# Kernel tuning notes

Hardware: AMD Instinct MI355X
Metric: run time of the kernel (lower is better)

The kernel has to match this reference:

```python
import jax, jax.numpy as jnp
import numpy as np

UNITS = 512
SENSORY = 256
BATCH = 256
ODE_UNFOLDS = 6
EPSILON = 1e-8
ELAPSED_TIME = 1.0


def setup_inputs() -> dict:
    key = jax.random.key(0)
    ks = jax.random.split(key, 16)
    u = lambda k, shape, lo, hi: jax.random.uniform(k, shape, jnp.float32, lo, hi)
    pm1 = lambda k, shape: (jax.random.randint(k, shape, 0, 2).astype(jnp.float32) * 2.0 - 1.0)
    return {
        "x": jax.random.normal(ks[0], (BATCH, SENSORY), jnp.float32),
        "state": jax.random.normal(ks[1], (BATCH, UNITS), jnp.float32),
        "gleak": u(ks[2], (UNITS,), 0.001, 1.0),
        "vleak": u(ks[3], (UNITS,), -0.2, 0.2),
        "cm": u(ks[4], (UNITS,), 0.4, 0.6),
        "sigma": u(ks[5], (UNITS, UNITS), 3.0, 8.0),
        "mu": u(ks[6], (UNITS, UNITS), 0.3, 0.8),
        "w": u(ks[7], (UNITS, UNITS), 0.001, 1.0),
        "erev": pm1(ks[8], (UNITS, UNITS)),
        "sensory_sigma": u(ks[9], (SENSORY, UNITS), 3.0, 8.0),
        "sensory_mu": u(ks[10], (SENSORY, UNITS), 0.3, 0.8),
        "sensory_w": u(ks[11], (SENSORY, UNITS), 0.001, 1.0),
        "sensory_erev": pm1(ks[12], (SENSORY, UNITS)),
        "input_w": jnp.ones((SENSORY,), jnp.float32),
        "input_b": jnp.zeros((SENSORY,), jnp.float32),
        "output_w": jnp.ones((UNITS,), jnp.float32),
        "output_b": jnp.zeros((UNITS,), jnp.float32),
    }


def _gate(v_pre, mu, sigma):
    # v_pre: (B, P) broadcast against (P, Q) params -> (B, P, Q)
    return jax.nn.sigmoid(sigma * (v_pre[:, :, None] - mu))


def reference(x, state, gleak, vleak, cm, sigma, mu, w, erev,
              sensory_sigma, sensory_mu, sensory_w, sensory_erev,
              input_w, input_b, output_w, output_b):
    inputs = x * input_w + input_b  # (B, D)
    sens_act = sensory_w * _gate(inputs, sensory_mu, sensory_sigma)  # (B, D, N)
    w_num_sensory = jnp.sum(sens_act * sensory_erev, axis=1)  # (B, N)
    w_den_sensory = jnp.sum(sens_act, axis=1)                 # (B, N)

    cm_t = cm / ((ELAPSED_TIME + 0.001) / ODE_UNFOLDS)  # (N,)
    v_pre = state
    for _ in range(ODE_UNFOLDS):
        w_act = w * _gate(v_pre, mu, sigma)               # (B, N, N)
        w_num = jnp.sum(w_act * erev, axis=1) + w_num_sensory
        w_den = jnp.sum(w_act, axis=1) + w_den_sensory
        numerator = cm_t * v_pre + gleak * vleak + w_num
        denominator = cm_t + gleak + w_den
        v_pre = numerator / (denominator + EPSILON)

    outputs = v_pre * output_w + output_b
    return outputs, v_pre
```

## Files before the change

### kernel.cpp

```cpp
#include <hip/hip_runtime.h>

#define UNITS 512
#define SENSD 256
#define BATCH 256
#define BN (BATCH * UNITS)
#define LOG2E 1.44269504088896340736f
#define CMF (6.0f / 1.001f)

__device__ __forceinline__ float frcp(float x)  { return __builtin_amdgcn_rcpf(x); }
__device__ __forceinline__ float fexp2(float x) { return __builtin_amdgcn_exp2f(x); }

__global__ __launch_bounds__(256) void prep_kernel(
    const float* __restrict__ sigma, const float* __restrict__ mu,
    const float* __restrict__ w, const float* __restrict__ erev,
    const float* __restrict__ ssig, const float* __restrict__ smu,
    const float* __restrict__ sw, const float* __restrict__ serev,
    const float* __restrict__ gleak, const float* __restrict__ vleak,
    const float* __restrict__ cm,
    float4* __restrict__ fusedR, float4* __restrict__ fusedS,
    float4* __restrict__ cmg) {
  int idx = blockIdx.x * 256 + threadIdx.x;
  if (idx < UNITS * UNITS) {
    float s = sigma[idx], m = mu[idx], ww = w[idx], e = erev[idx];
    fusedR[idx] = make_float4(-s * LOG2E, s * m * LOG2E, ww, ww * e);
  } else {
    int j = idx - UNITS * UNITS;
    if (j < SENSD * UNITS) {
      float s = ssig[j], m = smu[j], ww = sw[j], e = serev[j];
      fusedS[j] = make_float4(-s * LOG2E, s * m * LOG2E, ww, ww * e);
    }
  }
  if (idx < UNITS) {
    float cmt = cm[idx] * CMF, gl = gleak[idx];
    cmg[idx] = make_float4(cmt, gl * vleak[idx], cmt + gl + 1e-8f, 0.f);
  }
}

__global__ __launch_bounds__(256, 2) void sensory_kernel(
    const float* __restrict__ x, const float* __restrict__ in_w, const float* __restrict__ in_b,
    const float4* __restrict__ fusedS,
    float* __restrict__ snf, float* __restrict__ sdf) {
  __shared__ float xl[128][20];
  int bi = blockIdx.x;
  int phs = bi & 1, qt = (bi >> 1) & 7, bt = bi >> 4;
  int tid = threadIdx.x;
  for (int i = tid; i < 2048; i += 256) {
    int br = i >> 7, dl = i & 127;
    int d = phs * 128 + dl;
    xl[dl][br] = fmaf(x[(bt * 16 + br) * SENSD + d], in_w[d], in_b[d]);
  }
  __syncthreads();
  int ql = tid & 63, bg = tid >> 6;
  int q = qt * 64 + ql;
  int r0 = bg * 4;
  const float4* F = fusedS + (size_t)(phs * 128) * UNITS + q;
  float n0 = 0.f, n1 = 0.f, n2 = 0.f, n3 = 0.f;
  float d0 = 0.f, d1 = 0.f, d2 = 0.f, d3 = 0.f;
  #pragma unroll 8
  for (int dd = 0; dd < 128; ++dd) {
    float4 f = F[(size_t)dd * UNITS];
    float4 vv = *(const float4*)&xl[dd][r0];
    float t0 = fexp2(fmaf(f.x, vv.x, f.y));
    float t1 = fexp2(fmaf(f.x, vv.y, f.y));
    float t2 = fexp2(fmaf(f.x, vv.z, f.y));
    float t3 = fexp2(fmaf(f.x, vv.w, f.y));
    float s0 = frcp(1.0f + t0);
    float s1 = frcp(1.0f + t1);
    float s2 = frcp(1.0f + t2);
    float s3 = frcp(1.0f + t3);
    n0 = fmaf(f.w, s0, n0);  d0 = fmaf(f.z, s0, d0);
    n1 = fmaf(f.w, s1, n1);  d1 = fmaf(f.z, s1, d1);
    n2 = fmaf(f.w, s2, n2);  d2 = fmaf(f.z, s2, d2);
    n3 = fmaf(f.w, s3, n3);  d3 = fmaf(f.z, s3, d3);
  }
  int bp = (bt * 16 + r0) * UNITS + q;
  size_t o = (size_t)phs * BN + bp;
  snf[o] = n0;             sdf[o] = d0;
  snf[o + UNITS] = n1;     sdf[o + UNITS] = d1;
  snf[o + 2 * UNITS] = n2; sdf[o + 2 * UNITS] = d2;
  snf[o + 3 * UNITS] = n3; sdf[o + 3 * UNITS] = d3;
}

__global__ __launch_bounds__(256, 2) void unfold_kernel(
    const float4* __restrict__ fusedR, const float* __restrict__ vprev,
    const float* __restrict__ pn_in, const float* __restrict__ pd_in,
    const float* __restrict__ snf, const float* __restrict__ sdf,
    const float4* __restrict__ cmg,
    float* __restrict__ vout,
    float* __restrict__ pn_out, float* __restrict__ pd_out,
    int first) {
  __shared__ float vl[128][20];
  int bi = blockIdx.x;
  int ph = bi & 3, qt = (bi >> 2) & 7, bt = bi >> 5;
  int tid = threadIdx.x;
  if (first) {
    for (int i = tid; i < 2048; i += 256) {
      int br = i >> 7, pl = i & 127;
      vl[pl][br] = vprev[(bt * 16 + br) * UNITS + ph * 128 + pl];
    }
  } else {
    for (int i = tid; i < 2048; i += 256) {
      int br = i >> 7, pl = i & 127;
      int p = ph * 128 + pl;
      int bp = (bt * 16 + br) * UNITS + p;
      float num = ((pn_in[bp] + pn_in[BN + bp]) + (pn_in[2 * BN + bp] + pn_in[3 * BN + bp]))
                + (snf[bp] + snf[BN + bp]);
      float den = ((pd_in[bp] + pd_in[BN + bp]) + (pd_in[2 * BN + bp] + pd_in[3 * BN + bp]))
                + (sdf[bp] + sdf[BN + bp]);
      float4 c = cmg[p];
      float v = fmaf(c.x, vprev[bp], c.y + num) * frcp(c.z + den);
      vl[pl][br] = v;
      if (qt == 0) vout[bp] = v;
    }
  }
  __syncthreads();
  int ql = tid & 63, bg = tid >> 6;
  int q = qt * 64 + ql;
  int r0 = bg * 4;
  const float4* F = fusedR + (size_t)(ph * 128) * UNITS + q;
  float n0 = 0.f, n1 = 0.f, n2 = 0.f, n3 = 0.f;
  float d0 = 0.f, d1 = 0.f, d2 = 0.f, d3 = 0.f;
  #pragma unroll 8
  for (int pp = 0; pp < 128; ++pp) {
    float4 f = F[(size_t)pp * UNITS];
    float4 vv = *(const float4*)&vl[pp][r0];
    float t0 = fexp2(fmaf(f.x, vv.x, f.y));
    float t1 = fexp2(fmaf(f.x, vv.y, f.y));
    float t2 = fexp2(fmaf(f.x, vv.z, f.y));
    float t3 = fexp2(fmaf(f.x, vv.w, f.y));
    float s0 = frcp(1.0f + t0);
    float s1 = frcp(1.0f + t1);
    float s2 = frcp(1.0f + t2);
    float s3 = frcp(1.0f + t3);
    n0 = fmaf(f.w, s0, n0);  d0 = fmaf(f.z, s0, d0);
    n1 = fmaf(f.w, s1, n1);  d1 = fmaf(f.z, s1, d1);
    n2 = fmaf(f.w, s2, n2);  d2 = fmaf(f.z, s2, d2);
    n3 = fmaf(f.w, s3, n3);  d3 = fmaf(f.z, s3, d3);
  }
  int bp = (bt * 16 + r0) * UNITS + q;
  size_t o = (size_t)ph * BN + bp;
  pn_out[o] = n0;             pd_out[o] = d0;
  pn_out[o + UNITS] = n1;     pd_out[o + UNITS] = d1;
  pn_out[o + 2 * UNITS] = n2; pd_out[o + 2 * UNITS] = d2;
  pn_out[o + 3 * UNITS] = n3; pd_out[o + 3 * UNITS] = d3;
}

__global__ __launch_bounds__(256) void final_kernel(
    const float* __restrict__ vprev,
    const float* __restrict__ pn, const float* __restrict__ pd,
    const float* __restrict__ snf, const float* __restrict__ sdf,
    const float4* __restrict__ cmg,
    const float* __restrict__ ow, const float* __restrict__ ob,
    float* __restrict__ out) {
  int idx = blockIdx.x * 256 + threadIdx.x;
  if (idx >= BN) return;
  int p = idx & (UNITS - 1);
  float num = ((pn[idx] + pn[BN + idx]) + (pn[2 * BN + idx] + pn[3 * BN + idx]))
            + (snf[idx] + snf[BN + idx]);
  float den = ((pd[idx] + pd[BN + idx]) + (pd[2 * BN + idx] + pd[3 * BN + idx]))
            + (sdf[idx] + sdf[BN + idx]);
  float4 c = cmg[p];
  float v = fmaf(c.x, vprev[idx], c.y + num) * frcp(c.z + den);
  out[idx] = fmaf(v, ow[p], ob[p]);
  out[BN + idx] = v;
}

extern "C" void kernel_launch(void* const* d_in, const int* in_sizes, int n_in,
                              void* d_out, int out_size, void* d_ws, size_t ws_size,
                              hipStream_t stream) {
  (void)in_sizes; (void)n_in; (void)out_size; (void)ws_size;
  const float* x     = (const float*)d_in[0];
  const float* state = (const float*)d_in[1];
  const float* gleak = (const float*)d_in[2];
  const float* vleak = (const float*)d_in[3];
  const float* cm    = (const float*)d_in[4];
  const float* sigma = (const float*)d_in[5];
  const float* mu    = (const float*)d_in[6];
  const float* w     = (const float*)d_in[7];
  const float* erev  = (const float*)d_in[8];
  const float* ssig  = (const float*)d_in[9];
  const float* smu   = (const float*)d_in[10];
  const float* sw    = (const float*)d_in[11];
  const float* serev = (const float*)d_in[12];
  const float* in_w  = (const float*)d_in[13];
  const float* in_b  = (const float*)d_in[14];
  const float* out_w = (const float*)d_in[15];
  const float* out_b = (const float*)d_in[16];

  float* ws = (float*)d_ws;
  float4* fusedR = (float4*)(ws);
  float4* fusedS = (float4*)(ws + 1048576);
  float4* cmg    = (float4*)(ws + 1572864);
  float*  pnA    = ws + 1574912;
  float*  pdA    = ws + 2099200;
  float*  pnB    = ws + 2623488;
  float*  pdB    = ws + 3147776;
  float*  snf    = ws + 3672064;
  float*  sdf    = ws + 3934208;
  float*  vA     = ws + 4196352;
  float*  vB     = ws + 4327424;

  prep_kernel<<<1536, 256, 0, stream>>>(sigma, mu, w, erev, ssig, smu, sw, serev,
                                        gleak, vleak, cm, fusedR, fusedS, cmg);
  sensory_kernel<<<256, 256, 0, stream>>>(x, in_w, in_b, fusedS, snf, sdf);

  unfold_kernel<<<512, 256, 0, stream>>>(fusedR, state, pnA, pdA, snf, sdf, cmg,
                                         vA, pnA, pdA, 1);
  unfold_kernel<<<512, 256, 0, stream>>>(fusedR, state, pnA, pdA, snf, sdf, cmg,
                                         vA, pnB, pdB, 0);
  unfold_kernel<<<512, 256, 0, stream>>>(fusedR, vA, pnB, pdB, snf, sdf, cmg,
                                         vB, pnA, pdA, 0);
  unfold_kernel<<<512, 256, 0, stream>>>(fusedR, vB, pnA, pdA, snf, sdf, cmg,
                                         vA, pnB, pdB, 0);
  unfold_kernel<<<512, 256, 0, stream>>>(fusedR, vA, pnB, pdB, snf, sdf, cmg,
                                         vB, pnA, pdA, 0);
  unfold_kernel<<<512, 256, 0, stream>>>(fusedR, vB, pnA, pdA, snf, sdf, cmg,
                                         vA, pnB, pdB, 0);
  final_kernel<<<512, 256, 0, stream>>>(vA, pnB, pdB, snf, sdf, cmg,
                                        out_w, out_b, (float*)d_out);
}
```

Measured before the change: 196.4 us.

## Double grid parallelism by splitting reduction into 8 phases and halving sensory batch tile

The unfold kernel now splits the presynaptic reduction into 8 chunks of 64 instead of 4 chunks of 128, launching 1024 blocks with a higher occupancy hint, and the partial-sum buffers grow to 8 slices that are summed in the next step. The sensory kernel processes 8 batch rows per block with 2 rows per thread, doubling its block count. The goal is to fill the many compute units of the GPU better on this small problem. The cost is more partial-sum traffic to global memory and extra reads when combining the slices.

```diff
diff --git a/kernel.cpp b/kernel.cpp
--- a/kernel.cpp
+++ b/kernel.cpp
@@ -36,52 +36,43 @@
   }
 }
 
-__global__ __launch_bounds__(256, 2) void sensory_kernel(
+__global__ __launch_bounds__(256) void sensory_kernel(
     const float* __restrict__ x, const float* __restrict__ in_w, const float* __restrict__ in_b,
     const float4* __restrict__ fusedS,
     float* __restrict__ snf, float* __restrict__ sdf) {
-  __shared__ float xl[128][20];
+  __shared__ float xl[8][128];
   int bi = blockIdx.x;
   int phs = bi & 1, qt = (bi >> 1) & 7, bt = bi >> 4;
   int tid = threadIdx.x;
-  for (int i = tid; i < 2048; i += 256) {
+  for (int i = tid; i < 1024; i += 256) {
     int br = i >> 7, dl = i & 127;
     int d = phs * 128 + dl;
-    xl[dl][br] = fmaf(x[(bt * 16 + br) * SENSD + d], in_w[d], in_b[d]);
+    xl[br][dl] = fmaf(x[(bt * 8 + br) * SENSD + d], in_w[d], in_b[d]);
   }
   __syncthreads();
   int ql = tid & 63, bg = tid >> 6;
   int q = qt * 64 + ql;
-  int r0 = bg * 4;
+  int r0 = bg * 2;
   const float4* F = fusedS + (size_t)(phs * 128) * UNITS + q;
-  float n0 = 0.f, n1 = 0.f, n2 = 0.f, n3 = 0.f;
-  float d0 = 0.f, d1 = 0.f, d2 = 0.f, d3 = 0.f;
+  float n0 = 0.f, dn0 = 0.f, n1 = 0.f, dn1 = 0.f;
   #pragma unroll 8
   for (int dd = 0; dd < 128; ++dd) {
     float4 f = F[(size_t)dd * UNITS];
-    float4 vv = *(const float4*)&xl[dd][r0];
-    float t0 = fexp2(fmaf(f.x, vv.x, f.y));
-    float t1 = fexp2(fmaf(f.x, vv.y, f.y));
-    float t2 = fexp2(fmaf(f.x, vv.z, f.y));
-    float t3 = fexp2(fmaf(f.x, vv.w, f.y));
+    float v0 = xl[r0][dd], v1 = xl[r0 + 1][dd];
+    float t0 = fexp2(fmaf(f.x, v0, f.y));
+    float t1 = fexp2(fmaf(f.x, v1, f.y));
     float s0 = frcp(1.0f + t0);
     float s1 = frcp(1.0f + t1);
-    float s2 = frcp(1.0f + t2);
-    float s3 = frcp(1.0f + t3);
-    n0 = fmaf(f.w, s0, n0);  d0 = fmaf(f.z, s0, d0);
-    n1 = fmaf(f.w, s1, n1);  d1 = fmaf(f.z, s1, d1);
-    n2 = fmaf(f.w, s2, n2);  d2 = fmaf(f.z, s2, d2);
-    n3 = fmaf(f.w, s3, n3);  d3 = fmaf(f.z, s3, d3);
-  }
-  int bp = (bt * 16 + r0) * UNITS + q;
-  size_t o = (size_t)phs * BN + bp;
-  snf[o] = n0;             sdf[o] = d0;
-  snf[o + UNITS] = n1;     sdf[o + UNITS] = d1;
-  snf[o + 2 * UNITS] = n2; sdf[o + 2 * UNITS] = d2;
-  snf[o + 3 * UNITS] = n3; sdf[o + 3 * UNITS] = d3;
-}
-
-__global__ __launch_bounds__(256, 2) void unfold_kernel(
+    n0 = fmaf(f.w, s0, n0);  dn0 = fmaf(f.z, s0, dn0);
+    n1 = fmaf(f.w, s1, n1);  dn1 = fmaf(f.z, s1, dn1);
+  }
+  int bp0 = (bt * 8 + r0) * UNITS + q;
+  size_t o = (size_t)phs * BN + bp0;
+  snf[o] = n0;         sdf[o] = dn0;
+  snf[o + UNITS] = n1; sdf[o + UNITS] = dn1;
+}
+
+__global__ __launch_bounds__(256, 4) void unfold_kernel(
     const float4* __restrict__ fusedR, const float* __restrict__ vprev,
     const float* __restrict__ pn_in, const float* __restrict__ pd_in,
     const float* __restrict__ snf, const float* __restrict__ sdf,
@@ -89,23 +80,25 @@
     float* __restrict__ vout,
     float* __restrict__ pn_out, float* __restrict__ pd_out,
     int first) {
-  __shared__ float vl[128][20];
+  __shared__ float vl[64][20];
   int bi = blockIdx.x;
-  int ph = bi & 3, qt = (bi >> 2) & 7, bt = bi >> 5;
+  int ph = bi & 7, qt = (bi >> 3) & 7, bt = bi >> 6;
   int tid = threadIdx.x;
   if (first) {
-    for (int i = tid; i < 2048; i += 256) {
-      int br = i >> 7, pl = i & 127;
-      vl[pl][br] = vprev[(bt * 16 + br) * UNITS + ph * 128 + pl];
+    for (int i = tid; i < 1024; i += 256) {
+      int br = i >> 6, pl = i & 63;
+      vl[pl][br] = vprev[(bt * 16 + br) * UNITS + ph * 64 + pl];
     }
   } else {
-    for (int i = tid; i < 2048; i += 256) {
-      int br = i >> 7, pl = i & 127;
-      int p = ph * 128 + pl;
+    for (int i = tid; i < 1024; i += 256) {
+      int br = i >> 6, pl = i & 63;
+      int p = ph * 64 + pl;
       int bp = (bt * 16 + br) * UNITS + p;
       float num = ((pn_in[bp] + pn_in[BN + bp]) + (pn_in[2 * BN + bp] + pn_in[3 * BN + bp]))
+                + ((pn_in[4 * BN + bp] + pn_in[5 * BN + bp]) + (pn_in[6 * BN + bp] + pn_in[7 * BN + bp]))
                 + (snf[bp] + snf[BN + bp]);
       float den = ((pd_in[bp] + pd_in[BN + bp]) + (pd_in[2 * BN + bp] + pd_in[3 * BN + bp]))
+                + ((pd_in[4 * BN + bp] + pd_in[5 * BN + bp]) + (pd_in[6 * BN + bp] + pd_in[7 * BN + bp]))
                 + (sdf[bp] + sdf[BN + bp]);
       float4 c = cmg[p];
       float v = fmaf(c.x, vprev[bp], c.y + num) * frcp(c.z + den);
@@ -117,11 +110,11 @@
   int ql = tid & 63, bg = tid >> 6;
   int q = qt * 64 + ql;
   int r0 = bg * 4;
-  const float4* F = fusedR + (size_t)(ph * 128) * UNITS + q;
+  const float4* F = fusedR + (size_t)(ph * 64) * UNITS + q;
   float n0 = 0.f, n1 = 0.f, n2 = 0.f, n3 = 0.f;
   float d0 = 0.f, d1 = 0.f, d2 = 0.f, d3 = 0.f;
   #pragma unroll 8
-  for (int pp = 0; pp < 128; ++pp) {
+  for (int pp = 0; pp < 64; ++pp) {
     float4 f = F[(size_t)pp * UNITS];
     float4 vv = *(const float4*)&vl[pp][r0];
     float t0 = fexp2(fmaf(f.x, vv.x, f.y));
@@ -156,8 +149,10 @@
   if (idx >= BN) return;
   int p = idx & (UNITS - 1);
   float num = ((pn[idx] + pn[BN + idx]) + (pn[2 * BN + idx] + pn[3 * BN + idx]))
+            + ((pn[4 * BN + idx] + pn[5 * BN + idx]) + (pn[6 * BN + idx] + pn[7 * BN + idx]))
             + (snf[idx] + snf[BN + idx]);
   float den = ((pd[idx] + pd[BN + idx]) + (pd[2 * BN + idx] + pd[3 * BN + idx]))
+            + ((pd[4 * BN + idx] + pd[5 * BN + idx]) + (pd[6 * BN + idx] + pd[7 * BN + idx]))
             + (sdf[idx] + sdf[BN + idx]);
   float4 c = cmg[p];
   float v = fmaf(c.x, vprev[idx], c.y + num) * frcp(c.z + den);
@@ -192,30 +187,30 @@
   float4* fusedS = (float4*)(ws + 1048576);
   float4* cmg    = (float4*)(ws + 1572864);
   float*  pnA    = ws + 1574912;
-  float*  pdA    = ws + 2099200;
-  float*  pnB    = ws + 2623488;
-  float*  pdB    = ws + 3147776;
-  float*  snf    = ws + 3672064;
-  float*  sdf    = ws + 3934208;
-  float*  vA     = ws + 4196352;
-  float*  vB     = ws + 4327424;
+  float*  pdA    = ws + 2623488;
+  float*  pnB    = ws + 3672064;
+  float*  pdB    = ws + 4720640;
+  float*  snf    = ws + 5769216;
+  float*  sdf    = ws + 6031360;
+  float*  vA     = ws + 6293504;
+  float*  vB     = ws + 6424576;
 
   prep_kernel<<<1536, 256, 0, stream>>>(sigma, mu, w, erev, ssig, smu, sw, serev,
                                         gleak, vleak, cm, fusedR, fusedS, cmg);
-  sensory_kernel<<<256, 256, 0, stream>>>(x, in_w, in_b, fusedS, snf, sdf);
-
-  unfold_kernel<<<512, 256, 0, stream>>>(fusedR, state, pnA, pdA, snf, sdf, cmg,
-                                         vA, pnA, pdA, 1);
-  unfold_kernel<<<512, 256, 0, stream>>>(fusedR, state, pnA, pdA, snf, sdf, cmg,
-                                         vA, pnB, pdB, 0);
-  unfold_kernel<<<512, 256, 0, stream>>>(fusedR, vA, pnB, pdB, snf, sdf, cmg,
-                                         vB, pnA, pdA, 0);
-  unfold_kernel<<<512, 256, 0, stream>>>(fusedR, vB, pnA, pdA, snf, sdf, cmg,
-                                         vA, pnB, pdB, 0);
-  unfold_kernel<<<512, 256, 0, stream>>>(fusedR, vA, pnB, pdB, snf, sdf, cmg,
-                                         vB, pnA, pdA, 0);
-  unfold_kernel<<<512, 256, 0, stream>>>(fusedR, vB, pnA, pdA, snf, sdf, cmg,
-                                         vA, pnB, pdB, 0);
+  sensory_kernel<<<512, 256, 0, stream>>>(x, in_w, in_b, fusedS, snf, sdf);
+
+  unfold_kernel<<<1024, 256, 0, stream>>>(fusedR, state, pnA, pdA, snf, sdf, cmg,
+                                          vA, pnA, pdA, 1);
+  unfold_kernel<<<1024, 256, 0, stream>>>(fusedR, state, pnA, pdA, snf, sdf, cmg,
+                                          vA, pnB, pdB, 0);
+  unfold_kernel<<<1024, 256, 0, stream>>>(fusedR, vA, pnB, pdB, snf, sdf, cmg,
+                                          vB, pnA, pdA, 0);
+  unfold_kernel<<<1024, 256, 0, stream>>>(fusedR, vB, pnA, pdA, snf, sdf, cmg,
+                                          vA, pnB, pdB, 0);
+  unfold_kernel<<<1024, 256, 0, stream>>>(fusedR, vA, pnB, pdB, snf, sdf, cmg,
+                                          vB, pnA, pdA, 0);
+  unfold_kernel<<<1024, 256, 0, stream>>>(fusedR, vB, pnA, pdA, snf, sdf, cmg,
+                                          vA, pnB, pdB, 0);
   final_kernel<<<512, 256, 0, stream>>>(vA, pnB, pdB, snf, sdf, cmg,
                                         out_w, out_b, (float*)d_out);
 }
```

Result: faster. 158.2 us (-19.4%).
